# Performance work log

Hardware: AMD Instinct MI355X
Metric: run time of the kernel (lower is better)

Reference implementation:

```python
import jax, jax.numpy as jnp
import numpy as np


def setup_inputs() -> dict:
    key = jax.random.key(0)
    kq, kk, kv = jax.random.split(key, 3)
    B, Hq, Hkv, S, D = 2, 16, 4, 2048, 64
    q = jax.random.normal(kq, (B, Hq, S, D), dtype=jnp.float32)
    k = jax.random.normal(kk, (B, Hkv, S, D), dtype=jnp.float32)
    v = jax.random.normal(kv, (B, Hkv, S, D), dtype=jnp.float32)
    return {"q": q, "k": k, "v": v}


def reference(q, k, v):
    # SDPA MATH backend: softmax(q k^T * scale) v, with GQA head repetition.
    Hq = q.shape[1]
    Hkv = k.shape[1]
    rep = Hq // Hkv
    if rep > 1:
        k = jnp.repeat(k, rep, axis=1)  # [B,Hq,S,D]
        v = jnp.repeat(v, rep, axis=1)
    scale = 1.0 / jnp.sqrt(jnp.asarray(q.shape[-1], dtype=q.dtype))
    scores = jnp.einsum("bhqd,bhkd->bhqk", q, k) * scale  # [B,Hq,S,S]
    attn = jax.nn.softmax(scores, axis=-1)
    return jnp.einsum("bhqk,bhkd->bhqd", attn, v)
```

## Files before the change

kernel.cpp:

```cpp
#include <hip/hip_runtime.h>
#include <hip/hip_bf16.h>

typedef unsigned short u16;
typedef short s16x4 __attribute__((ext_vector_type(4)));
typedef short s16x8 __attribute__((ext_vector_type(8)));
typedef float fx4 __attribute__((ext_vector_type(4)));
typedef unsigned ux2 __attribute__((ext_vector_type(2)));

#define BATCH 2
#define NHQ 16
#define NHKV 4
#define SEQ 2048
#define HD 64
#define TM 128
#define TN 128
#define NTILES (SEQ / TN)
#define VSTRIDE 132
#define NKV (BATCH * NHKV * SEQ * HD)
#define QSCALE 0.18033688011112042f

__device__ __forceinline__ unsigned pack2_bf16(float a, float b) {
    const unsigned ua = __float_as_uint(a) + 0x8000u;
    const unsigned ub = __float_as_uint(b) + 0x8000u;
    return __builtin_amdgcn_perm(ub, ua, 0x07060302u);
}
__device__ __forceinline__ unsigned ilv_lo(unsigned r0, unsigned r1) {
    return __builtin_amdgcn_perm(r1, r0, 0x05040100u);
}
__device__ __forceinline__ unsigned ilv_hi(unsigned r0, unsigned r1) {
    return __builtin_amdgcn_perm(r1, r0, 0x07060302u);
}

__global__ __launch_bounds__(256) void cvt_kv_kernel(
    const float* __restrict__ K, const float* __restrict__ V,
    u16* __restrict__ wsK, u16* __restrict__ wsV)
{
    const int i = (blockIdx.x * 256 + threadIdx.x) * 4;
    const fx4 k4 = *(const fx4*)(K + i);
    const fx4 v4 = *(const fx4*)(V + i);
    ux2 ko, vo;
    ko[0] = pack2_bf16(k4[0], k4[1]);
    ko[1] = pack2_bf16(k4[2], k4[3]);
    vo[0] = pack2_bf16(v4[0], v4[1]);
    vo[1] = pack2_bf16(v4[2], v4[3]);
    *(ux2*)(wsK + i) = ko;
    *(ux2*)(wsV + i) = vo;
}

__global__ __launch_bounds__(512, 4) void ptSDPA_39668317946373_kernel(
    const float* __restrict__ gQ,
    const u16* __restrict__ wsK,
    const u16* __restrict__ wsV,
    float* __restrict__ gO)
{
    __shared__ u16 shK[2][TN * HD];
    __shared__ u16 shVt[2][HD * VSTRIDE];

    const int tid = threadIdx.x;
    const int wv  = tid >> 6;
    const int ln  = tid & 63;
    const int l15 = ln & 15;
    const int qd  = ln >> 4;

    const int g     = blockIdx.x;
    const int kvg   = g & 7;
    const int inner = g >> 3;
    const int qtb   = inner & 15;
    const int hqw   = inner >> 4;
    const int batch = kvg >> 2;
    const int hkv   = kvg & 3;
    const int head  = batch * NHQ + hkv * 4 + hqw;

    const int t0 = (inner & 3) * 4;

    const float* q_base = gQ + (size_t)head * SEQ * HD;
    const u16*   k_base = wsK + (size_t)kvg * SEQ * HD;
    const u16*   v_base = wsV + (size_t)kvg * SEQ * HD;
    float*       o_base = gO + (size_t)head * SEQ * HD;

    const int qrow0 = qtb * TM;

    const bool isC = (wv < 4);

    s16x8 qfrag[2][2];
    fx4 oacc[2][4];
    fx4 racc[2];
    const fx4 z4 = {0.f, 0.f, 0.f, 0.f};
#pragma unroll
    for (int mi = 0; mi < 2; mi++) {
        racc[mi] = z4;
#pragma unroll
        for (int ni = 0; ni < 4; ni++) oacc[mi][ni] = z4;
    }
    const s16x8 ones8 = {(short)0x3F80, (short)0x3F80, (short)0x3F80,
                         (short)0x3F80, (short)0x3F80, (short)0x3F80,
                         (short)0x3F80, (short)0x3F80};

    if (isC) {
#pragma unroll
        for (int mi = 0; mi < 2; mi++) {
            const int row = qrow0 + wv * 32 + mi * 16 + l15;
#pragma unroll
            for (int ks = 0; ks < 2; ks++) {
                const int d0 = ks * 32 + qd * 8;
                const fx4 lo = *(const fx4*)(q_base + (size_t)row * HD + d0);
                const fx4 hi = *(const fx4*)(q_base + (size_t)row * HD + d0 + 4);
                union { unsigned u[4]; s16x8 v; } t;
                t.u[0] = pack2_bf16(lo[0] * QSCALE, lo[1] * QSCALE);
                t.u[1] = pack2_bf16(lo[2] * QSCALE, lo[3] * QSCALE);
                t.u[2] = pack2_bf16(hi[0] * QSCALE, hi[1] * QSCALE);
                t.u[3] = pack2_bf16(hi[2] * QSCALE, hi[3] * QSCALE);
                qfrag[mi][ks] = t.v;
            }
        }
    }

    const int st = tid - 256;
    const int skey  = st & 127;
    const int shalf = st >> 7;
    const u16* kp0 = k_base + skey * HD + shalf * 32;
    const int vkey = (st & 63) * 2;
    const int vd0  = (st >> 6) * 16;
    const u16* vp0 = v_base + vkey * HD + vd0;

    if (!isC) {
        s16x8 kreg[4], vreg[4];
        const u16* kp = kp0 + (size_t)t0 * TN * HD;
        const u16* vp = vp0 + (size_t)t0 * TN * HD;
#pragma unroll
        for (int s = 0; s < 4; s++) kreg[s] = *(const s16x8*)(kp + s * 8);
        vreg[0] = *(const s16x8*)(vp);
        vreg[1] = *(const s16x8*)(vp + 8);
        vreg[2] = *(const s16x8*)(vp + HD);
        vreg[3] = *(const s16x8*)(vp + HD + 8);
#pragma unroll
        for (int s = 0; s < 4; s++) {
            const int c = shalf * 4 + s;
            *(s16x8*)(shK[0] + skey * 64 + ((c ^ (skey & 7)) * 8)) = kreg[s];
        }
#pragma unroll
        for (int h = 0; h < 2; h++) {
            union { s16x8 v; unsigned u[4]; } r0, r1;
            r0.v = vreg[h];
            r1.v = vreg[2 + h];
#pragma unroll
            for (int c2 = 0; c2 < 4; c2++) {
                const int d = vd0 + h * 8 + c2 * 2;
                *(unsigned*)(shVt[0] + d * VSTRIDE + vkey) =
                    ilv_lo(r0.u[c2], r1.u[c2]);
                *(unsigned*)(shVt[0] + (d + 1) * VSTRIDE + vkey) =
                    ilv_hi(r0.u[c2], r1.u[c2]);
            }
        }
    }

#pragma unroll 2
    for (int i = 0; i < NTILES; i++) {
        const int cur = i & 1;
        const int nxt = cur ^ 1;

        __syncthreads();

        if (isC) {
            const int kb7 = l15 & 7;
            const int sw0 = (qd ^ kb7) << 3;
            const int sw1 = ((4 + qd) ^ kb7) << 3;
            const u16* kRow = shK[cur] + l15 * 64;

            fx4 scp[2][2][2];
#pragma unroll
            for (int kt2 = 0; kt2 < 2; kt2++) {
                const s16x8 kf0 = *(const s16x8*)(kRow + kt2 * 1024 + sw0);
                const s16x8 kf1 = *(const s16x8*)(kRow + kt2 * 1024 + sw1);
#pragma unroll
                for (int mi = 0; mi < 2; mi++) {
                    fx4 s = __builtin_amdgcn_mfma_f32_16x16x32_bf16(
                        kf0, qfrag[mi][0], z4, 0, 0, 0);
                    s = __builtin_amdgcn_mfma_f32_16x16x32_bf16(
                        kf1, qfrag[mi][1], s, 0, 0, 0);
                    scp[0][kt2][mi] = s;
                }
            }

#pragma unroll
            for (int jp = 0; jp < 4; jp++) {
                const int pp = jp & 1;
                if (jp < 3) {
#pragma unroll
                    for (int kt2 = 0; kt2 < 2; kt2++) {
                        const int kt = (jp + 1) * 2 + kt2;
                        const s16x8 kf0 =
                            *(const s16x8*)(kRow + kt * 1024 + sw0);
                        const s16x8 kf1 =
                            *(const s16x8*)(kRow + kt * 1024 + sw1);
#pragma unroll
                        for (int mi = 0; mi < 2; mi++) {
                            fx4 s = __builtin_amdgcn_mfma_f32_16x16x32_bf16(
                                kf0, qfrag[mi][0], z4, 0, 0, 0);
                            s = __builtin_amdgcn_mfma_f32_16x16x32_bf16(
                                kf1, qfrag[mi][1], s, 0, 0, 0);
                            scp[pp ^ 1][kt2][mi] = s;
                        }
                    }
                }

                const int kbase = jp * 32 + qd * 4;
                s16x8 vf8[4];
#pragma unroll
                for (int ni = 0; ni < 4; ni++) {
                    const u16* row = shVt[cur] + (ni * 16 + l15) * VSTRIDE;
                    union { s16x4 h[2]; s16x8 v; } u;
                    u.h[0] = *(const s16x4*)(row + kbase);
                    u.h[1] = *(const s16x4*)(row + kbase + 16);
                    vf8[ni] = u.v;
                }

                s16x8 af[2];
#pragma unroll
                for (int mi = 0; mi < 2; mi++) {
                    const float e0 = __builtin_amdgcn_exp2f(scp[pp][0][mi][0]);
                    const float e1 = __builtin_amdgcn_exp2f(scp[pp][0][mi][1]);
                    const float e2 = __builtin_amdgcn_exp2f(scp[pp][0][mi][2]);
                    const float e3 = __builtin_amdgcn_exp2f(scp[pp][0][mi][3]);
                    const float f0 = __builtin_amdgcn_exp2f(scp[pp][1][mi][0]);
                    const float f1 = __builtin_amdgcn_exp2f(scp[pp][1][mi][1]);
                    const float f2 = __builtin_amdgcn_exp2f(scp[pp][1][mi][2]);
                    const float f3 = __builtin_amdgcn_exp2f(scp[pp][1][mi][3]);
                    union { unsigned u[4]; s16x8 v; } pk;
                    pk.u[0] = pack2_bf16(e0, e1);
                    pk.u[1] = pack2_bf16(e2, e3);
                    pk.u[2] = pack2_bf16(f0, f1);
                    pk.u[3] = pack2_bf16(f2, f3);
                    af[mi] = pk.v;
                }

#pragma unroll
                for (int mi = 0; mi < 2; mi++)
                    racc[mi] = __builtin_amdgcn_mfma_f32_16x16x32_bf16(
                        af[mi], ones8, racc[mi], 0, 0, 0);

#pragma unroll
                for (int ni = 0; ni < 4; ni++) {
#pragma unroll
                    for (int mi = 0; mi < 2; mi++)
                        oacc[mi][ni] = __builtin_amdgcn_mfma_f32_16x16x32_bf16(
                            af[mi], vf8[ni], oacc[mi][ni], 0, 0, 0);
                }
            }
        } else {
            if (i + 1 < NTILES) {
                const int tp = (t0 + i + 1) & (NTILES - 1);
                s16x8 kreg[4], vreg[4];
                const u16* kp = kp0 + (size_t)tp * TN * HD;
                const u16* vp = vp0 + (size_t)tp * TN * HD;
#pragma unroll
                for (int s = 0; s < 4; s++)
                    kreg[s] = *(const s16x8*)(kp + s * 8);
                vreg[0] = *(const s16x8*)(vp);
                vreg[1] = *(const s16x8*)(vp + 8);
                vreg[2] = *(const s16x8*)(vp + HD);
                vreg[3] = *(const s16x8*)(vp + HD + 8);
#pragma unroll
                for (int s = 0; s < 4; s++) {
                    const int c = shalf * 4 + s;
                    *(s16x8*)(shK[nxt] + skey * 64 + ((c ^ (skey & 7)) * 8)) =
                        kreg[s];
                }
#pragma unroll
                for (int h = 0; h < 2; h++) {
                    union { s16x8 v; unsigned u[4]; } r0, r1;
                    r0.v = vreg[h];
                    r1.v = vreg[2 + h];
#pragma unroll
                    for (int c2 = 0; c2 < 4; c2++) {
                        const int d = vd0 + h * 8 + c2 * 2;
                        *(unsigned*)(shVt[nxt] + d * VSTRIDE + vkey) =
                            ilv_lo(r0.u[c2], r1.u[c2]);
                        *(unsigned*)(shVt[nxt] + (d + 1) * VSTRIDE + vkey) =
                            ilv_hi(r0.u[c2], r1.u[c2]);
                    }
                }
            }
        }
    }

    if (isC) {
#pragma unroll
        for (int mi = 0; mi < 2; mi++) {
            float inv[4];
#pragma unroll
            for (int r = 0; r < 4; r++) inv[r] = 1.0f / racc[mi][r];
#pragma unroll
            for (int ni = 0; ni < 4; ni++)
#pragma unroll
                for (int r = 0; r < 4; r++) {
                    const int qr = qrow0 + wv * 32 + mi * 16 + qd * 4 + r;
                    o_base[(size_t)qr * HD + ni * 16 + l15] =
                        oacc[mi][ni][r] * inv[r];
                }
        }
    }
}

extern "C" void kernel_launch(void* const* d_in, const int* in_sizes, int n_in,
                              void* d_out, int out_size, void* d_ws, size_t ws_size,
                              hipStream_t stream) {
    const float* q = (const float*)d_in[0];
    const float* k = (const float*)d_in[1];
    const float* v = (const float*)d_in[2];
    float*       o = (float*)d_out;
    u16* wsK = (u16*)d_ws;
    u16* wsV = wsK + NKV;
    cvt_kv_kernel<<<NKV / 1024, 256, 0, stream>>>(k, v, wsK, wsV);
    const dim3 grid(BATCH * NHQ * (SEQ / TM));
    ptSDPA_39668317946373_kernel<<<grid, 512, 0, stream>>>(q, wsK, wsV, o);
}
```

Before: 115.6 us.

## Halve block to 4 waves with 64 query rows per compute wave

Shrinks the block from 8 waves (4 compute, 4 loader) to 4 waves (2 compute, 2 loader). Each compute wave now handles 64 query rows instead of 32, so every K/V fragment read from shared memory feeds twice as many MFMAs. Each loader thread moves twice as much K/V data per tile. The V-fragment loads are hoisted ahead of the score MFMAs and the exp/PV loop is fused per row block. In exchange there are fewer waves per block for latency hiding, register pressure is higher, and the per-tile staging work is serialized over fewer threads.

Measured after the change: 131.9 us. 1.14x slower.

```diff
diff --git a/kernel.cpp b/kernel.cpp
--- a/kernel.cpp
+++ b/kernel.cpp
@@ -47,7 +47,7 @@
     *(ux2*)(wsV + i) = vo;
 }
 
-__global__ __launch_bounds__(512, 4) void ptSDPA_39668317946373_kernel(
+__global__ __launch_bounds__(256, 2) void ptSDPA_39668317946373_kernel(
     const float* __restrict__ gQ,
     const u16* __restrict__ wsK,
     const u16* __restrict__ wsV,
@@ -80,14 +80,14 @@
 
     const int qrow0 = qtb * TM;
 
-    const bool isC = (wv < 4);
-
-    s16x8 qfrag[2][2];
-    fx4 oacc[2][4];
-    fx4 racc[2];
+    const bool isC = (wv < 2);
+
+    s16x8 qfrag[4][2];
+    fx4 oacc[4][4];
+    fx4 racc[4];
     const fx4 z4 = {0.f, 0.f, 0.f, 0.f};
 #pragma unroll
-    for (int mi = 0; mi < 2; mi++) {
+    for (int mi = 0; mi < 4; mi++) {
         racc[mi] = z4;
 #pragma unroll
         for (int ni = 0; ni < 4; ni++) oacc[mi][ni] = z4;
@@ -98,8 +98,8 @@
 
     if (isC) {
 #pragma unroll
-        for (int mi = 0; mi < 2; mi++) {
-            const int row = qrow0 + wv * 32 + mi * 16 + l15;
+        for (int mi = 0; mi < 4; mi++) {
+            const int row = qrow0 + wv * 64 + mi * 16 + l15;
 #pragma unroll
             for (int ks = 0; ks < 2; ks++) {
                 const int d0 = ks * 32 + qd * 8;
@@ -115,34 +115,32 @@
         }
     }
 
-    const int st = tid - 256;
-    const int skey  = st & 127;
-    const int shalf = st >> 7;
-    const u16* kp0 = k_base + skey * HD + shalf * 32;
+    const int st = tid - 128;
+    const int skey = st & 127;
+    const u16* kp0 = k_base + skey * HD;
     const int vkey = (st & 63) * 2;
-    const int vd0  = (st >> 6) * 16;
+    const int vd0  = (st >> 6) * 32;
     const u16* vp0 = v_base + vkey * HD + vd0;
 
     if (!isC) {
-        s16x8 kreg[4], vreg[4];
+        s16x8 kreg[8], vreg[8];
         const u16* kp = kp0 + (size_t)t0 * TN * HD;
         const u16* vp = vp0 + (size_t)t0 * TN * HD;
 #pragma unroll
-        for (int s = 0; s < 4; s++) kreg[s] = *(const s16x8*)(kp + s * 8);
-        vreg[0] = *(const s16x8*)(vp);
-        vreg[1] = *(const s16x8*)(vp + 8);
-        vreg[2] = *(const s16x8*)(vp + HD);
-        vreg[3] = *(const s16x8*)(vp + HD + 8);
+        for (int s = 0; s < 8; s++) kreg[s] = *(const s16x8*)(kp + s * 8);
 #pragma unroll
         for (int s = 0; s < 4; s++) {
-            const int c = shalf * 4 + s;
-            *(s16x8*)(shK[0] + skey * 64 + ((c ^ (skey & 7)) * 8)) = kreg[s];
-        }
-#pragma unroll
-        for (int h = 0; h < 2; h++) {
+            vreg[s]     = *(const s16x8*)(vp + s * 8);
+            vreg[4 + s] = *(const s16x8*)(vp + HD + s * 8);
+        }
+#pragma unroll
+        for (int c = 0; c < 8; c++)
+            *(s16x8*)(shK[0] + skey * 64 + ((c ^ (skey & 7)) * 8)) = kreg[c];
+#pragma unroll
+        for (int h = 0; h < 4; h++) {
             union { s16x8 v; unsigned u[4]; } r0, r1;
             r0.v = vreg[h];
-            r1.v = vreg[2 + h];
+            r1.v = vreg[4 + h];
 #pragma unroll
             for (int c2 = 0; c2 < 4; c2++) {
                 const int d = vd0 + h * 8 + c2 * 2;
@@ -167,13 +165,13 @@
             const int sw1 = ((4 + qd) ^ kb7) << 3;
             const u16* kRow = shK[cur] + l15 * 64;
 
-            fx4 scp[2][2][2];
+            fx4 scp[2][2][4];
 #pragma unroll
             for (int kt2 = 0; kt2 < 2; kt2++) {
                 const s16x8 kf0 = *(const s16x8*)(kRow + kt2 * 1024 + sw0);
                 const s16x8 kf1 = *(const s16x8*)(kRow + kt2 * 1024 + sw1);
 #pragma unroll
-                for (int mi = 0; mi < 2; mi++) {
+                for (int mi = 0; mi < 4; mi++) {
                     fx4 s = __builtin_amdgcn_mfma_f32_16x16x32_bf16(
                         kf0, qfrag[mi][0], z4, 0, 0, 0);
                     s = __builtin_amdgcn_mfma_f32_16x16x32_bf16(
@@ -185,6 +183,18 @@
 #pragma unroll
             for (int jp = 0; jp < 4; jp++) {
                 const int pp = jp & 1;
+
+                const int kbase = jp * 32 + qd * 4;
+                s16x8 vf8[4];
+#pragma unroll
+                for (int ni = 0; ni < 4; ni++) {
+                    const u16* row = shVt[cur] + (ni * 16 + l15) * VSTRIDE;
+                    union { s16x4 h[2]; s16x8 v; } u;
+                    u.h[0] = *(const s16x4*)(row + kbase);
+                    u.h[1] = *(const s16x4*)(row + kbase + 16);
+                    vf8[ni] = u.v;
+                }
+
                 if (jp < 3) {
 #pragma unroll
                     for (int kt2 = 0; kt2 < 2; kt2++) {
@@ -194,7 +204,7 @@
                         const s16x8 kf1 =
                             *(const s16x8*)(kRow + kt * 1024 + sw1);
 #pragma unroll
-                        for (int mi = 0; mi < 2; mi++) {
+                        for (int mi = 0; mi < 4; mi++) {
                             fx4 s = __builtin_amdgcn_mfma_f32_16x16x32_bf16(
                                 kf0, qfrag[mi][0], z4, 0, 0, 0);
                             s = __builtin_amdgcn_mfma_f32_16x16x32_bf16(
@@ -204,20 +214,8 @@
                     }
                 }
 
-                const int kbase = jp * 32 + qd * 4;
-                s16x8 vf8[4];
-#pragma unroll
-                for (int ni = 0; ni < 4; ni++) {
-                    const u16* row = shVt[cur] + (ni * 16 + l15) * VSTRIDE;
-                    union { s16x4 h[2]; s16x8 v; } u;
-                    u.h[0] = *(const s16x4*)(row + kbase);
-                    u.h[1] = *(const s16x4*)(row + kbase + 16);
-                    vf8[ni] = u.v;
-                }
-
-                s16x8 af[2];
-#pragma unroll
-                for (int mi = 0; mi < 2; mi++) {
+#pragma unroll
+                for (int mi = 0; mi < 4; mi++) {
                     const float e0 = __builtin_amdgcn_exp2f(scp[pp][0][mi][0]);
                     const float e1 = __builtin_amdgcn_exp2f(scp[pp][0][mi][1]);
                     const float e2 = __builtin_amdgcn_exp2f(scp[pp][0][mi][2]);
@@ -231,46 +229,39 @@
                     pk.u[1] = pack2_bf16(e2, e3);
                     pk.u[2] = pack2_bf16(f0, f1);
                     pk.u[3] = pack2_bf16(f2, f3);
-                    af[mi] = pk.v;
-                }
-
-#pragma unroll
-                for (int mi = 0; mi < 2; mi++)
+                    const s16x8 af = pk.v;
+
                     racc[mi] = __builtin_amdgcn_mfma_f32_16x16x32_bf16(
-                        af[mi], ones8, racc[mi], 0, 0, 0);
-
-#pragma unroll
-                for (int ni = 0; ni < 4; ni++) {
-#pragma unroll
-                    for (int mi = 0; mi < 2; mi++)
+                        af, ones8, racc[mi], 0, 0, 0);
+#pragma unroll
+                    for (int ni = 0; ni < 4; ni++)
                         oacc[mi][ni] = __builtin_amdgcn_mfma_f32_16x16x32_bf16(
-                            af[mi], vf8[ni], oacc[mi][ni], 0, 0, 0);
+                            af, vf8[ni], oacc[mi][ni], 0, 0, 0);
                 }
             }
         } else {
             if (i + 1 < NTILES) {
                 const int tp = (t0 + i + 1) & (NTILES - 1);
-                s16x8 kreg[4], vreg[4];
+                s16x8 kreg[8], vreg[8];
                 const u16* kp = kp0 + (size_t)tp * TN * HD;
                 const u16* vp = vp0 + (size_t)tp * TN * HD;
 #pragma unroll
-                for (int s = 0; s < 4; s++)
+                for (int s = 0; s < 8; s++)
                     kreg[s] = *(const s16x8*)(kp + s * 8);
-                vreg[0] = *(const s16x8*)(vp);
-                vreg[1] = *(const s16x8*)(vp + 8);
-                vreg[2] = *(const s16x8*)(vp + HD);
-                vreg[3] = *(const s16x8*)(vp + HD + 8);
 #pragma unroll
                 for (int s = 0; s < 4; s++) {
-                    const int c = shalf * 4 + s;
+                    vreg[s]     = *(const s16x8*)(vp + s * 8);
+                    vreg[4 + s] = *(const s16x8*)(vp + HD + s * 8);
+                }
+#pragma unroll
+                for (int c = 0; c < 8; c++)
                     *(s16x8*)(shK[nxt] + skey * 64 + ((c ^ (skey & 7)) * 8)) =
-                        kreg[s];
-                }
-#pragma unroll
-                for (int h = 0; h < 2; h++) {
+                        kreg[c];
+#pragma unroll
+                for (int h = 0; h < 4; h++) {
                     union { s16x8 v; unsigned u[4]; } r0, r1;
                     r0.v = vreg[h];
-                    r1.v = vreg[2 + h];
+                    r1.v = vreg[4 + h];
 #pragma unroll
                     for (int c2 = 0; c2 < 4; c2++) {
                         const int d = vd0 + h * 8 + c2 * 2;
@@ -286,7 +277,7 @@
 
     if (isC) {
 #pragma unroll
-        for (int mi = 0; mi < 2; mi++) {
+        for (int mi = 0; mi < 4; mi++) {
             float inv[4];
 #pragma unroll
             for (int r = 0; r < 4; r++) inv[r] = 1.0f / racc[mi][r];
@@ -294,7 +285,7 @@
             for (int ni = 0; ni < 4; ni++)
 #pragma unroll
                 for (int r = 0; r < 4; r++) {
-                    const int qr = qrow0 + wv * 32 + mi * 16 + qd * 4 + r;
+                    const int qr = qrow0 + wv * 64 + mi * 16 + qd * 4 + r;
                     o_base[(size_t)qr * HD + ni * 16 + l15] =
                         oacc[mi][ni][r] * inv[r];
                 }
@@ -313,5 +304,5 @@
     u16* wsV = wsK + NKV;
     cvt_kv_kernel<<<NKV / 1024, 256, 0, stream>>>(k, v, wsK, wsV);
     const dim3 grid(BATCH * NHQ * (SEQ / TM));
-    ptSDPA_39668317946373_kernel<<<grid, 512, 0, stream>>>(q, wsK, wsV, o);
-}
+    ptSDPA_39668317946373_kernel<<<grid, 256, 0, stream>>>(q, wsK, wsV, o);
+}
```
